# Kernel optimization log

Hardware: AMD Instinct MI355X
Metric: run time of the kernel (lower is better)

Reference implementation:

```python
import jax, jax.numpy as jnp
import numpy as np

NUM_NODES = 100000
NUM_EDGES = 1600000
NUM_GRAPHS = 64
IN_DIM, HID, NCLS = 64, 128, 10


def setup_inputs() -> dict:
    key = jax.random.key(0)
    ks = jax.random.split(key, 12)
    x = jax.random.normal(ks[0], (NUM_NODES, IN_DIM), dtype=jnp.float32)
    src = jax.random.randint(ks[1], (NUM_EDGES,), 0, NUM_NODES, dtype=jnp.int32)
    dst = jax.random.randint(ks[2], (NUM_EDGES,), 0, NUM_NODES, dtype=jnp.int32)
    batch = jnp.sort(jax.random.randint(ks[3], (NUM_NODES,), 0, NUM_GRAPHS, dtype=jnp.int32))
    def glorot(k, shape):
        lim = (6.0 / (shape[0] + shape[1])) ** 0.5
        return jax.random.uniform(k, shape, jnp.float32, -lim, lim)
    return {
        "x": x, "src": src, "dst": dst, "batch": batch,
        "W1": glorot(ks[4], (IN_DIM, HID)), "b1": jnp.zeros((HID,), jnp.float32),
        "W2": glorot(ks[5], (HID, HID)), "b2": jnp.zeros((HID,), jnp.float32),
        "Wl1": glorot(ks[6], (HID, HID // 2)), "bl1": jnp.zeros((HID // 2,), jnp.float32),
        "Wl2": glorot(ks[7], (HID // 2, NCLS)), "bl2": jnp.zeros((NCLS,), jnp.float32),
    }


def gcn_conv(x, W, b, src, dst):
    # GCNConv: out = D^{-1/2} (A + I) D^{-1/2} (x @ W) + b, deg from A+I
    h = x @ W  # [N, H]
    ones = jnp.ones((src.shape[0],), h.dtype)
    deg = jax.ops.segment_sum(ones, dst, num_segments=NUM_NODES) + 1.0  # +1 self-loop
    dinv = jax.lax.rsqrt(deg)  # [N]
    norm = dinv[src] * dinv[dst]  # [E]
    msg = h[src] * norm[:, None]  # [E, H] gather + scale
    agg = jax.ops.segment_sum(msg, dst, num_segments=NUM_NODES)  # scatter-add
    agg = agg + h * (dinv * dinv)[:, None]  # self-loop message
    return agg + b


def reference(x, src, dst, batch, W1, b1, W2, b2, Wl1, bl1, Wl2, bl2):
    h = jax.nn.relu(gcn_conv(x, W1, b1, src, dst))
    h = jax.nn.relu(gcn_conv(h, W2, b2, src, dst))
    # global mean pool per graph
    sums = jax.ops.segment_sum(h, batch, num_segments=NUM_GRAPHS)  # [G, H]
    cnts = jax.ops.segment_sum(jnp.ones((h.shape[0],), h.dtype), batch, num_segments=NUM_GRAPHS)
    pooled = sums / jnp.maximum(cnts, 1.0)[:, None]
    h = jax.nn.relu(pooled @ Wl1 + bl1)
    return h @ Wl2 + bl2  # [G, num_classes]
```

## Files before the change

kernel.cpp:

```cpp
#include <hip/hip_runtime.h>
#include <hip/hip_bf16.h>

#define NODES_N 100000
#define EDGES_E 1600000
#define GRAPHS_G 64

#define BIN_SHIFT 7
#define BIN_NODES 128
#define NBINS 782
#define NB1 512
#define EPB1 3125

typedef unsigned int uint;
typedef unsigned short ushort;
typedef __attribute__((ext_vector_type(8))) short bf16x8;
typedef __attribute__((ext_vector_type(4))) float f32x4;


__device__ inline uint pack_bf2(float lo, float hi) {
    __hip_bfloat162 h2 = __float22bfloat162_rn(make_float2(lo, hi));
    return *reinterpret_cast<uint*>(&h2);
}

__device__ inline void acc_bf2(uint w, float& a0, float& a1) {
    a0 += __uint_as_float(w << 16);
    a1 += __uint_as_float(w & 0xffff0000u);
}

__device__ inline ushort f2bf(float v) {
    __hip_bfloat16 b = __float2bfloat16(v);
    return *reinterpret_cast<ushort*>(&b);
}


__device__ inline void pack_w_one(const float* W, ushort* Wf, int gid, int KS) {
    int j = gid & 7, l = (gid >> 3) & 63, f = gid >> 9;
    int nt = f / KS, ks = f - nt * KS;
    int k = ks * 32 + ((l >> 4) & 3) * 8 + j;
    int n = nt * 16 + (l & 15);
    Wf[gid] = f2bf(W[k * 128 + n]);
}

__global__ void pack_w_zero_k(const float* __restrict__ W1, ushort* __restrict__ W1f,
                              const float* __restrict__ W2, ushort* __restrict__ W2f,
                              float* __restrict__ zf) {
    int gid = blockIdx.x * 256 + threadIdx.x;
    if (gid < 8192) pack_w_one(W1, W1f, gid, 2);
    else if (gid < 24576) pack_w_one(W2, W2f, gid - 8192, 4);
    else {
        int i = gid - 24576;
        if (i < GRAPHS_G * 128 + GRAPHS_G) zf[i] = 0.f;
    }
}


__global__ __launch_bounds__(256) void p1_hist_k(const int* __restrict__ dst,
                                                 int* __restrict__ hist_t) {
    __shared__ int h[NBINS];
    for (int i = threadIdx.x; i < NBINS; i += 256) h[i] = 0;
    __syncthreads();
    int b = blockIdx.x;
    int e0 = b * EPB1, e1 = min(EDGES_E, e0 + EPB1);
    for (int e = e0 + threadIdx.x; e < e1; e += 256)
        atomicAdd(&h[dst[e] >> BIN_SHIFT], 1);
    __syncthreads();
    for (int i = threadIdx.x; i < NBINS; i += 256)
        hist_t[i * NB1 + b] = h[i];
}

__global__ __launch_bounds__(256) void p1_scanbins_k(int* __restrict__ hist_t,
                                                     int* __restrict__ bintot) {
    __shared__ int sd[256];
    __shared__ int carry;
    int bin = blockIdx.x, t = threadIdx.x;
    if (t == 0) carry = 0;
    __syncthreads();
    int* row = hist_t + bin * NB1;
    for (int base = 0; base < NB1; base += 256) {
        int v = row[base + t];
        sd[t] = v; __syncthreads();
        for (int o = 1; o < 256; o <<= 1) {
            int x = (t >= o) ? sd[t - o] : 0;
            __syncthreads();
            sd[t] += x;
            __syncthreads();
        }
        row[base + t] = carry + sd[t] - v;
        __syncthreads();
        if (t == 255) carry += sd[255];
        __syncthreads();
    }
    if (t == 0) bintot[bin] = carry;
}

__global__ __launch_bounds__(1024) void binstart_k(const int* __restrict__ bintot,
                                                   int* __restrict__ binstart,
                                                   int* __restrict__ rowptr) {
    __shared__ int sd[1024];
    int t = threadIdx.x;
    int v = (t < NBINS) ? bintot[t] : 0;
    sd[t] = v; __syncthreads();
    for (int o = 1; o < 1024; o <<= 1) {
        int x = (t >= o) ? sd[t - o] : 0;
        __syncthreads();
        sd[t] += x;
        __syncthreads();
    }
    if (t < NBINS) binstart[t] = sd[t] - v;
    if (t == 0) { binstart[NBINS] = EDGES_E; rowptr[NODES_N] = EDGES_E; }
}

__global__ __launch_bounds__(256) void p1_scatter_k(const int* __restrict__ src,
                                                    const int* __restrict__ dst,
                                                    const int* __restrict__ hist_t,
                                                    const int* __restrict__ binstart,
                                                    uint* __restrict__ pairs) {
    __shared__ int cur[NBINS];
    int b = blockIdx.x;
    for (int i = threadIdx.x; i < NBINS; i += 256)
        cur[i] = binstart[i] + hist_t[i * NB1 + b];
    __syncthreads();
    int e0 = b * EPB1, e1 = min(EDGES_E, e0 + EPB1);
    for (int e = e0 + threadIdx.x; e < e1; e += 256) {
        int d = dst[e];
        int pos = atomicAdd(&cur[d >> BIN_SHIFT], 1);
        pairs[pos] = ((uint)src[e] << BIN_SHIFT) | (uint)(d & (BIN_NODES - 1));
    }
}

__global__ __launch_bounds__(256) void p2_build_k(const uint* __restrict__ pairs,
                                                  const int* __restrict__ binstart,
                                                  const float* __restrict__ x,
                                                  int* __restrict__ colidx,
                                                  int* __restrict__ rowptr,
                                                  float* __restrict__ dinv,
                                                  uint* __restrict__ xt) {
    __shared__ int h[BIN_NODES];
    __shared__ int off[BIN_NODES];
    __shared__ int cur[BIN_NODES];
    __shared__ float ldv[BIN_NODES];
    int bin = blockIdx.x, t = threadIdx.x;
    int node0 = bin << BIN_SHIFT;
    if (t < BIN_NODES) h[t] = 0;
    __syncthreads();
    int e0 = binstart[bin], e1 = binstart[bin + 1];
    for (int e = e0 + t; e < e1; e += 256)
        atomicAdd(&h[pairs[e] & (BIN_NODES - 1)], 1);
    __syncthreads();
    if (t < BIN_NODES) off[t] = h[t];
    __syncthreads();
    for (int o = 1; o < BIN_NODES; o <<= 1) {
        int x2 = (t < BIN_NODES && t >= o) ? off[t - o] : 0;
        __syncthreads();
        if (t < BIN_NODES) off[t] += x2;
        __syncthreads();
    }
    if (t < BIN_NODES) {
        int excl = off[t] - h[t];
        cur[t] = e0 + excl;
        float dv = rsqrtf((float)h[t] + 1.0f);
        ldv[t] = dv;
        int node = node0 + t;
        if (node < NODES_N) {
            rowptr[node] = e0 + excl;
            dinv[node] = dv;
        }
    }
    __syncthreads();
    for (int e = e0 + t; e < e1; e += 256) {
        uint p = pairs[e];
        int pos = atomicAdd(&cur[p & (BIN_NODES - 1)], 1);
        colidx[pos] = (int)(p >> BIN_SHIFT);
    }
    int nmax = min(NODES_N - node0, BIN_NODES);
    for (int i = t; i < nmax * 16; i += 256) {
        int nl = i >> 4, c = i & 15;
        int node = node0 + nl;
        float dv = ldv[nl];
        float4 v = *(const float4*)&x[(size_t)node * 64 + c * 4];
        uint2 o = make_uint2(pack_bf2(v.x * dv, v.y * dv), pack_bf2(v.z * dv, v.w * dv));
        *(uint2*)&xt[(size_t)node * 32 + c * 2] = o;
    }
}


__global__ __launch_bounds__(256) void conv1_fused_k(const uint* __restrict__ xt,
                                                     const int* __restrict__ rowptr,
                                                     const int* __restrict__ colidx,
                                                     const float* __restrict__ dinv,
                                                     const float* __restrict__ bias,
                                                     const ushort* __restrict__ Wf,
                                                     ushort* __restrict__ h1b, int n) {
    int wave = threadIdx.x >> 6;
    int lane = threadIdx.x & 63;
    int row0 = (blockIdx.x * 4 + wave) * 16;
    if (row0 >= n) return;
    int m = lane & 15, g = lane >> 4;
    int node = min(row0 + m, n - 1);
    int g4 = g * 4;

    float s[16];
#pragma unroll
    for (int i = 0; i < 16; i++) s[i] = 0.f;

    auto accrow = [&](int r) {
        uint4 vA = *(const uint4*)&xt[(size_t)r * 32 + g4];
        uint4 vB = *(const uint4*)&xt[(size_t)r * 32 + 16 + g4];
        acc_bf2(vA.x, s[0], s[1]);  acc_bf2(vA.y, s[2], s[3]);
        acc_bf2(vA.z, s[4], s[5]);  acc_bf2(vA.w, s[6], s[7]);
        acc_bf2(vB.x, s[8], s[9]);  acc_bf2(vB.y, s[10], s[11]);
        acc_bf2(vB.z, s[12], s[13]); acc_bf2(vB.w, s[14], s[15]);
    };

    accrow(node);
    int beg = rowptr[node], end = rowptr[node + 1];
    int e = beg;
    for (; e + 3 < end; e += 4) {
        int s0 = colidx[e], s1 = colidx[e + 1], s2 = colidx[e + 2], s3 = colidx[e + 3];
        accrow(s0); accrow(s1); accrow(s2); accrow(s3);
    }
    for (; e < end; e++) accrow(colidx[e]);

    uint4 u0 = make_uint4(pack_bf2(s[0], s[1]), pack_bf2(s[2], s[3]),
                          pack_bf2(s[4], s[5]), pack_bf2(s[6], s[7]));
    uint4 u1 = make_uint4(pack_bf2(s[8], s[9]), pack_bf2(s[10], s[11]),
                          pack_bf2(s[12], s[13]), pack_bf2(s[14], s[15]));
    bf16x8 a0 = *reinterpret_cast<bf16x8*>(&u0);
    bf16x8 a1 = *reinterpret_cast<bf16x8*>(&u1);

    f32x4 acc[8];
#pragma unroll
    for (int nt = 0; nt < 8; nt++) {
        acc[nt] = (f32x4){0.f, 0.f, 0.f, 0.f};
        bf16x8 b0 = *reinterpret_cast<const bf16x8*>(&Wf[((size_t)(nt * 2 + 0) * 64 + lane) * 8]);
        bf16x8 b1 = *reinterpret_cast<const bf16x8*>(&Wf[((size_t)(nt * 2 + 1) * 64 + lane) * 8]);
        acc[nt] = __builtin_amdgcn_mfma_f32_16x16x32_bf16(a0, b0, acc[nt], 0, 0, 0);
        acc[nt] = __builtin_amdgcn_mfma_f32_16x16x32_bf16(a1, b1, acc[nt], 0, 0, 0);
    }

    int orow0 = row0 + g * 4;
#pragma unroll
    for (int r = 0; r < 4; r++) {
        int row = orow0 + r;
        if (row < n) {
            float dvr = dinv[row];
#pragma unroll
            for (int nt = 0; nt < 8; nt++) {
                float v = fmaxf(fmaf(dvr, acc[nt][r], bias[nt * 16 + m]), 0.f);
                h1b[(size_t)row * 128 + nt * 16 + m] = f2bf(v);
            }
        }
    }
}


template <int K>
__global__ __launch_bounds__(256) void gemm_mfma_k(const ushort* __restrict__ A,
                                                   const ushort* __restrict__ Wf,
                                                   const float* __restrict__ dinv,
                                                   ushort* __restrict__ outb, int n) {
    constexpr int KS = K / 32;
    int wave = threadIdx.x >> 6;
    int lane = threadIdx.x & 63;
    int row0 = (blockIdx.x * 4 + wave) * 16;
    if (row0 >= n) return;
    int m = lane & 15, g = lane >> 4;
    int arow = min(row0 + m, n - 1);

    bf16x8 a[KS];
    const ushort* abase = &A[(size_t)arow * K + g * 8];
#pragma unroll
    for (int ks = 0; ks < KS; ks++)
        a[ks] = *reinterpret_cast<const bf16x8*>(abase + ks * 32);

    f32x4 acc[8];
#pragma unroll
    for (int nt = 0; nt < 8; nt++) {
        acc[nt] = (f32x4){0.f, 0.f, 0.f, 0.f};
#pragma unroll
        for (int ks = 0; ks < KS; ks++) {
            bf16x8 b = *reinterpret_cast<const bf16x8*>(&Wf[((size_t)(nt * KS + ks) * 64 + lane) * 8]);
            acc[nt] = __builtin_amdgcn_mfma_f32_16x16x32_bf16(a[ks], b, acc[nt], 0, 0, 0);
        }
    }

    int orow0 = row0 + g * 4;
#pragma unroll
    for (int r = 0; r < 4; r++) {
        int row = orow0 + r;
        if (row < n) {
            float dvr = dinv[row];
#pragma unroll
            for (int nt = 0; nt < 8; nt++)
                outb[(size_t)row * 128 + nt * 16 + m] = f2bf(acc[nt][r] * dvr);
        }
    }
}


template <int P>
__global__ __launch_bounds__(256) void gather128_k(const uint* __restrict__ hp,
                                                   const int* __restrict__ rowptr,
                                                   const int* __restrict__ colidx,
                                                   const float* __restrict__ dinv,
                                                   const float* __restrict__ bias,
                                                   uint* __restrict__ h2b, int n) {
    int lane = threadIdx.x & 7;
    int local = threadIdx.x >> 3;
    int co = P * 32 + lane * 4;
    for (int node = blockIdx.x * 32 + local; node < n; node += gridDim.x * 32) {
        float a0=0,a1=0,a2=0,a3=0,a4=0,a5=0,a6=0,a7=0;
        uint4 v = *(const uint4*)&hp[(size_t)node * 64 + co];
        acc_bf2(v.x, a0, a1); acc_bf2(v.y, a2, a3);
        acc_bf2(v.z, a4, a5); acc_bf2(v.w, a6, a7);
        int beg = rowptr[node], end = rowptr[node + 1];
        int e = beg;
        for (; e + 3 < end; e += 4) {
            int s0 = colidx[e], s1 = colidx[e+1], s2 = colidx[e+2], s3 = colidx[e+3];
            uint4 v0 = *(const uint4*)&hp[(size_t)s0 * 64 + co];
            uint4 v1 = *(const uint4*)&hp[(size_t)s1 * 64 + co];
            uint4 v2 = *(const uint4*)&hp[(size_t)s2 * 64 + co];
            uint4 v3 = *(const uint4*)&hp[(size_t)s3 * 64 + co];
            acc_bf2(v0.x,a0,a1); acc_bf2(v0.y,a2,a3); acc_bf2(v0.z,a4,a5); acc_bf2(v0.w,a6,a7);
            acc_bf2(v1.x,a0,a1); acc_bf2(v1.y,a2,a3); acc_bf2(v1.z,a4,a5); acc_bf2(v1.w,a6,a7);
            acc_bf2(v2.x,a0,a1); acc_bf2(v2.y,a2,a3); acc_bf2(v2.z,a4,a5); acc_bf2(v2.w,a6,a7);
            acc_bf2(v3.x,a0,a1); acc_bf2(v3.y,a2,a3); acc_bf2(v3.z,a4,a5); acc_bf2(v3.w,a6,a7);
        }
        for (; e < end; e++) {
            uint4 v0 = *(const uint4*)&hp[(size_t)colidx[e] * 64 + co];
            acc_bf2(v0.x,a0,a1); acc_bf2(v0.y,a2,a3); acc_bf2(v0.z,a4,a5); acc_bf2(v0.w,a6,a7);
        }
        float dv = dinv[node];
        int jb = P * 64 + lane * 8;
        float4 b0 = *(const float4*)&bias[jb];
        float4 b1 = *(const float4*)&bias[jb + 4];
        float o0 = fmaxf(fmaf(dv, a0, b0.x), 0.f);
        float o1 = fmaxf(fmaf(dv, a1, b0.y), 0.f);
        float o2 = fmaxf(fmaf(dv, a2, b0.z), 0.f);
        float o3 = fmaxf(fmaf(dv, a3, b0.w), 0.f);
        float o4 = fmaxf(fmaf(dv, a4, b1.x), 0.f);
        float o5 = fmaxf(fmaf(dv, a5, b1.y), 0.f);
        float o6 = fmaxf(fmaf(dv, a6, b1.z), 0.f);
        float o7 = fmaxf(fmaf(dv, a7, b1.w), 0.f);
        uint4 ov;
        ov.x = pack_bf2(o0, o1);
        ov.y = pack_bf2(o2, o3);
        ov.z = pack_bf2(o4, o5);
        ov.w = pack_bf2(o6, o7);
        *(uint4*)&h2b[(size_t)node * 64 + co] = ov;
    }
}


__global__ __launch_bounds__(128) void pool_k(const uint* __restrict__ h2b,
                                              const int* __restrict__ batch, int n,
                                              float* __restrict__ sums, float* __restrict__ cnts) {
    int j = threadIdx.x;
    int wj = j >> 1;
    int hi = j & 1;
    int chunk = (n + gridDim.x - 1) / gridDim.x;
    int i0 = blockIdx.x * chunk;
    int i1 = min(n, i0 + chunk);
    if (i0 >= n) return;
    int cur = batch[i0];
    float acc = 0.f;
    int cnt = 0;
    for (int i = i0; i < i1; i++) {
        int g = batch[i];
        if (g != cur) {
            atomicAdd(&sums[cur * 128 + j], acc);
            if (j == 0) atomicAdd(&cnts[cur], (float)cnt);
            acc = 0.f; cnt = 0; cur = g;
        }
        uint w = h2b[(size_t)i * 64 + wj];
        acc += __uint_as_float(hi ? (w & 0xffff0000u) : (w << 16));
        cnt++;
    }
    atomicAdd(&sums[cur * 128 + j], acc);
    if (j == 0) atomicAdd(&cnts[cur], (float)cnt);
}


__global__ __launch_bounds__(64) void mlp_k(const float* __restrict__ sums, const float* __restrict__ cnts,
                                            const float* __restrict__ Wl1, const float* __restrict__ bl1,
                                            const float* __restrict__ Wl2, const float* __restrict__ bl2,
                                            float* __restrict__ out) {
    __shared__ float pooled[128];
    __shared__ float hidden[64];
    int g = blockIdx.x, t = threadIdx.x;
    float c = fmaxf(cnts[g], 1.0f);
    pooled[t]      = sums[g * 128 + t] / c;
    pooled[t + 64] = sums[g * 128 + 64 + t] / c;
    __syncthreads();
    float a = bl1[t];
#pragma unroll 4
    for (int cc = 0; cc < 128; cc++) a = fmaf(pooled[cc], Wl1[cc * 64 + t], a);
    hidden[t] = fmaxf(a, 0.f);
    __syncthreads();
    if (t < 10) {
        float o = bl2[t];
#pragma unroll 8
        for (int jj = 0; jj < 64; jj++) o = fmaf(hidden[jj], Wl2[jj * 10 + t], o);
        out[g * 10 + t] = o;
    }
}


extern "C" void kernel_launch(void* const* d_in, const int* in_sizes, int n_in,
                              void* d_out, int out_size, void* d_ws, size_t ws_size,
                              hipStream_t stream) {
    const float* x    = (const float*)d_in[0];
    const int*   src  = (const int*)d_in[1];
    const int*   dst  = (const int*)d_in[2];
    const int*   batch= (const int*)d_in[3];
    const float* W1   = (const float*)d_in[4];
    const float* b1   = (const float*)d_in[5];
    const float* W2   = (const float*)d_in[6];
    const float* b2   = (const float*)d_in[7];
    const float* Wl1  = (const float*)d_in[8];
    const float* bl1  = (const float*)d_in[9];
    const float* Wl2  = (const float*)d_in[10];
    const float* bl2  = (const float*)d_in[11];
    float* out = (float*)d_out;

    const int N = NODES_N;

    size_t off = 0;
    auto take = [&](size_t bytes) { size_t o = off; off = (off + bytes + 255) & ~(size_t)255; return o; };
    char* ws = (char*)d_ws;
    ushort* h1b  = (ushort*)(ws + take((size_t)N * 128 * 2));
    uint*   h2p  = (uint*)(ws + take((size_t)N * 128 * 2));
    uint*   pairs = (uint*)(ws + take((size_t)EDGES_E * 4));
    uint*   xt   = (uint*)(ws + take((size_t)N * 64 * 2));
    float*  dinv = (float*)(ws + take((size_t)N * 4));
    ushort* W1f  = (ushort*)(ws + take((size_t)64 * 128 * 2));
    ushort* W2f  = (ushort*)(ws + take((size_t)128 * 128 * 2));
    size_t zbytes = ((size_t)GRAPHS_G * 128 + GRAPHS_G) * 4;
    char*  zbase  = ws + take(zbytes);
    float* sums   = (float*)zbase;
    float* cnts   = (float*)(zbase + (size_t)GRAPHS_G * 128 * 4);
    int*   rowptr = (int*)(ws + take((size_t)(N + 1) * 4));
    int*   colidx = (int*)(ws + take((size_t)EDGES_E * 4));
    int*   hist_t = (int*)(ws + take((size_t)NBINS * NB1 * 4));
    int*   bintot = (int*)(ws + take((size_t)NBINS * 4));
    int*   binstart = (int*)(ws + take((size_t)(NBINS + 1) * 4));
    uint*  h2b = (uint*)h1b;
    (void)ws_size; (void)in_sizes; (void)n_in; (void)out_size;

    pack_w_zero_k<<<(24576 + GRAPHS_G * 128 + GRAPHS_G + 255) / 256, 256, 0, stream>>>(
        W1, W1f, W2, W2f, sums);

    p1_hist_k<<<NB1, 256, 0, stream>>>(dst, hist_t);
    p1_scanbins_k<<<NBINS, 256, 0, stream>>>(hist_t, bintot);
    binstart_k<<<1, 1024, 0, stream>>>(bintot, binstart, rowptr);
    p1_scatter_k<<<NB1, 256, 0, stream>>>(src, dst, hist_t, binstart, pairs);
    p2_build_k<<<NBINS, 256, 0, stream>>>(pairs, binstart, x, colidx, rowptr, dinv, xt);

    int gblk = (N + 63) / 64;
    conv1_fused_k<<<gblk, 256, 0, stream>>>(xt, rowptr, colidx, dinv, b1, W1f, h1b, N);

    gemm_mfma_k<128><<<gblk, 256, 0, stream>>>(h1b, W2f, dinv, (ushort*)h2p, N);
    int g128 = (N + 31) / 32;
    gather128_k<0><<<g128, 256, 0, stream>>>(h2p, rowptr, colidx, dinv, b2, h2b, N);
    gather128_k<1><<<g128, 256, 0, stream>>>(h2p, rowptr, colidx, dinv, b2, h2b, N);

    pool_k<<<1024, 128, 0, stream>>>(h2b, batch, N, sums, cnts);
    mlp_k<<<GRAPHS_G, 64, 0, stream>>>(sums, cnts, Wl1, bl1, Wl2, bl2, out);
}
```

Measured before the change: 235.7 us.

## Split conv1 edge gather across two waves and fold binstart scan into last block

In conv1_fused_k, each 16-row tile is now handled by two waves, each taking half of every node's edge list. The partial sums are combined through shared memory before the MFMA step, which doubles the waves working on the latency-bound gather. Separately, the single-block binstart kernel is removed. The last-finishing block of p1_scanbins_k, found with an atomic counter, now does the bin prefix scan, saving one kernel launch. The costs are an extra block-level barrier and shared-memory reduction in conv1, plus a done counter that must be zeroed on every call.

After: 249.1 us. +5.7%, slower.

```diff
diff --git a/kernel.cpp b/kernel.cpp
--- a/kernel.cpp
+++ b/kernel.cpp
@@ -40,6 +40,8 @@
     int n = nt * 16 + (l & 15);
     Wf[gid] = f2bf(W[k * 128 + n]);
 }
+
+#define NZERO (GRAPHS_G * 128 + GRAPHS_G + 1)
 
 __global__ void pack_w_zero_k(const float* __restrict__ W1, ushort* __restrict__ W1f,
                               const float* __restrict__ W2, ushort* __restrict__ W2f,
@@ -49,7 +51,7 @@
     else if (gid < 24576) pack_w_one(W2, W2f, gid - 8192, 4);
     else {
         int i = gid - 24576;
-        if (i < GRAPHS_G * 128 + GRAPHS_G) zf[i] = 0.f;
+        if (i < NZERO) zf[i] = 0.f;
     }
 }
 
@@ -69,9 +71,13 @@
 }
 
 __global__ __launch_bounds__(256) void p1_scanbins_k(int* __restrict__ hist_t,
-                                                     int* __restrict__ bintot) {
+                                                     int* __restrict__ bintot,
+                                                     int* __restrict__ binstart,
+                                                     int* __restrict__ rowptr,
+                                                     int* __restrict__ done) {
     __shared__ int sd[256];
     __shared__ int carry;
+    __shared__ int last;
     int bin = blockIdx.x, t = threadIdx.x;
     if (t == 0) carry = 0;
     __syncthreads();
@@ -90,23 +96,31 @@
         if (t == 255) carry += sd[255];
         __syncthreads();
     }
-    if (t == 0) bintot[bin] = carry;
-}
-
-__global__ __launch_bounds__(1024) void binstart_k(const int* __restrict__ bintot,
-                                                   int* __restrict__ binstart,
-                                                   int* __restrict__ rowptr) {
-    __shared__ int sd[1024];
-    int t = threadIdx.x;
-    int v = (t < NBINS) ? bintot[t] : 0;
-    sd[t] = v; __syncthreads();
-    for (int o = 1; o < 1024; o <<= 1) {
-        int x = (t >= o) ? sd[t - o] : 0;
+    if (t == 0) {
+        __hip_atomic_store(&bintot[bin], carry, __ATOMIC_RELEASE, __HIP_MEMORY_SCOPE_AGENT);
+        int old = atomicAdd(done, 1);
+        last = (old == NBINS - 1) ? 1 : 0;
+    }
+    __syncthreads();
+    if (!last) return;
+    if (t == 0) carry = 0;
+    __syncthreads();
+    for (int base = 0; base < 1024; base += 256) {
+        int i = base + t;
+        int v = (i < NBINS)
+              ? __hip_atomic_load(&bintot[i], __ATOMIC_ACQUIRE, __HIP_MEMORY_SCOPE_AGENT) : 0;
+        sd[t] = v; __syncthreads();
+        for (int o = 1; o < 256; o <<= 1) {
+            int x = (t >= o) ? sd[t - o] : 0;
+            __syncthreads();
+            sd[t] += x;
+            __syncthreads();
+        }
+        if (i < NBINS) binstart[i] = carry + sd[t] - v;
         __syncthreads();
-        sd[t] += x;
+        if (t == 255) carry += sd[255];
         __syncthreads();
     }
-    if (t < NBINS) binstart[t] = sd[t] - v;
     if (t == 0) { binstart[NBINS] = EDGES_E; rowptr[NODES_N] = EDGES_E; }
 }
 
@@ -191,13 +205,15 @@
                                                      const float* __restrict__ bias,
                                                      const ushort* __restrict__ Wf,
                                                      ushort* __restrict__ h1b, int n) {
+    __shared__ float part[2][16][64];
     int wave = threadIdx.x >> 6;
     int lane = threadIdx.x & 63;
-    int row0 = (blockIdx.x * 4 + wave) * 16;
-    if (row0 >= n) return;
+    int tt = wave >> 1;
+    int ab = wave & 1;
+    int row0 = (blockIdx.x * 2 + tt) * 16;
     int m = lane & 15, g = lane >> 4;
-    int node = min(row0 + m, n - 1);
     int g4 = g * 4;
+    bool active = row0 < n;
 
     float s[16];
 #pragma unroll
@@ -212,14 +228,31 @@
         acc_bf2(vB.z, s[12], s[13]); acc_bf2(vB.w, s[14], s[15]);
     };
 
-    accrow(node);
-    int beg = rowptr[node], end = rowptr[node + 1];
-    int e = beg;
-    for (; e + 3 < end; e += 4) {
-        int s0 = colidx[e], s1 = colidx[e + 1], s2 = colidx[e + 2], s3 = colidx[e + 3];
-        accrow(s0); accrow(s1); accrow(s2); accrow(s3);
-    }
-    for (; e < end; e++) accrow(colidx[e]);
+    int node = 0;
+    if (active) {
+        node = min(row0 + m, n - 1);
+        int beg = rowptr[node], end = rowptr[node + 1];
+        int half = (end - beg + 1) >> 1;
+        int e0 = ab ? beg + half : beg;
+        int e1 = ab ? end : beg + half;
+        if (ab == 0) accrow(node);
+        int e = e0;
+        for (; e + 3 < e1; e += 4) {
+            int s0 = colidx[e], s1 = colidx[e + 1], s2 = colidx[e + 2], s3 = colidx[e + 3];
+            accrow(s0); accrow(s1); accrow(s2); accrow(s3);
+        }
+        for (; e < e1; e++) accrow(colidx[e]);
+    }
+
+    if (ab == 1) {
+#pragma unroll
+        for (int i = 0; i < 16; i++) part[tt][i][lane] = s[i];
+    }
+    __syncthreads();
+    if (ab == 1 || !active) return;
+
+#pragma unroll
+    for (int i = 0; i < 16; i++) s[i] += part[tt][i][lane];
 
     uint4 u0 = make_uint4(pack_bf2(s[0], s[1]), pack_bf2(s[2], s[3]),
                           pack_bf2(s[4], s[5]), pack_bf2(s[6], s[7]));
@@ -435,10 +468,11 @@
     float*  dinv = (float*)(ws + take((size_t)N * 4));
     ushort* W1f  = (ushort*)(ws + take((size_t)64 * 128 * 2));
     ushort* W2f  = (ushort*)(ws + take((size_t)128 * 128 * 2));
-    size_t zbytes = ((size_t)GRAPHS_G * 128 + GRAPHS_G) * 4;
+    size_t zbytes = (size_t)NZERO * 4;
     char*  zbase  = ws + take(zbytes);
     float* sums   = (float*)zbase;
     float* cnts   = (float*)(zbase + (size_t)GRAPHS_G * 128 * 4);
+    int*   done   = (int*)(zbase + (size_t)(GRAPHS_G * 128 + GRAPHS_G) * 4);
     int*   rowptr = (int*)(ws + take((size_t)(N + 1) * 4));
     int*   colidx = (int*)(ws + take((size_t)EDGES_E * 4));
     int*   hist_t = (int*)(ws + take((size_t)NBINS * NB1 * 4));
@@ -447,18 +481,17 @@
     uint*  h2b = (uint*)h1b;
     (void)ws_size; (void)in_sizes; (void)n_in; (void)out_size;
 
-    pack_w_zero_k<<<(24576 + GRAPHS_G * 128 + GRAPHS_G + 255) / 256, 256, 0, stream>>>(
-        W1, W1f, W2, W2f, sums);
+    pack_w_zero_k<<<(24576 + NZERO + 255) / 256, 256, 0, stream>>>(W1, W1f, W2, W2f, sums);
 
     p1_hist_k<<<NB1, 256, 0, stream>>>(dst, hist_t);
-    p1_scanbins_k<<<NBINS, 256, 0, stream>>>(hist_t, bintot);
-    binstart_k<<<1, 1024, 0, stream>>>(bintot, binstart, rowptr);
+    p1_scanbins_k<<<NBINS, 256, 0, stream>>>(hist_t, bintot, binstart, rowptr, done);
     p1_scatter_k<<<NB1, 256, 0, stream>>>(src, dst, hist_t, binstart, pairs);
     p2_build_k<<<NBINS, 256, 0, stream>>>(pairs, binstart, x, colidx, rowptr, dinv, xt);
 
+    int c1blk = (N + 31) / 32;
+    conv1_fused_k<<<c1blk, 256, 0, stream>>>(xt, rowptr, colidx, dinv, b1, W1f, h1b, N);
+
     int gblk = (N + 63) / 64;
-    conv1_fused_k<<<gblk, 256, 0, stream>>>(xt, rowptr, colidx, dinv, b1, W1f, h1b, N);
-
     gemm_mfma_k<128><<<gblk, 256, 0, stream>>>(h1b, W2f, dinv, (ushort*)h2p, N);
     int g128 = (N + 31) / 32;
     gather128_k<0><<<g128, 256, 0, stream>>>(h2p, rowptr, colidx, dinv, b2, h2b, N);
```
